# Kernel tuning notes

Measured on AMD Instinct MI355X. Metric: run time of the kernel, lower is better.

The kernel has to match this reference:

```python
import jax, jax.numpy as jnp
import numpy as np

B, L, HID, H, D = 1, 2048, 3072, 24, 128
MLP = 4 * HID
LH, LW = 32, 56      # latent mask grid -> LH*LW image tokens at the END of the sequence
LIP = 16             # IP-adapter image tokens
IP_SCALE = 0.6


def setup_inputs() -> dict:
    key = jax.random.key(0)
    k = jax.random.split(key, 10)
    # Flux rotary pe layout [1,1,L,D//2,2,2]: pe[...,0]=[cos,-sin], pe[...,1]=[sin,cos]
    pos = jnp.arange(L, dtype=jnp.float32)
    freqs = 1.0 / (10000.0 ** (jnp.arange(0, D, 2, dtype=jnp.float32) / D))
    ang = pos[:, None] * freqs[None, :]            # [L, D//2]
    cos, sin = jnp.cos(ang), jnp.sin(ang)
    pe = jnp.stack([jnp.stack([cos, -sin], -1), jnp.stack([sin, cos], -1)], -2)[None, None]
    return {
        "x": jax.random.normal(k[0], (B, L, HID), jnp.float32),
        "vec": jax.random.normal(k[1], (B, HID), jnp.float32),
        "pe": pe,
        "img_mask": jax.random.uniform(k[2], (B, LH, LW), jnp.float32),
        "image_emb": jax.random.normal(k[3], (B, LIP, HID), jnp.float32),
        "mod_w": jax.random.normal(k[4], (3 * HID, HID), jnp.float32) * 0.02,
        "mod_b": jnp.zeros((3 * HID,), jnp.float32),
        "lin1_w": jax.random.normal(k[5], (3 * HID + MLP, HID), jnp.float32) * 0.02,
        "lin1_b": jnp.zeros((3 * HID + MLP,), jnp.float32),
        "q_scale": jnp.ones((D,), jnp.float32),
        "k_scale": jnp.ones((D,), jnp.float32),
        "lin2_w": jax.random.normal(k[6], (HID, HID + MLP), jnp.float32) * 0.02,
        "lin2_b": jnp.zeros((HID,), jnp.float32),
        "ipk_w": jax.random.normal(k[7], (HID, HID), jnp.float32) * 0.02,
        "ipv_w": jax.random.normal(k[8], (HID, HID), jnp.float32) * 0.02,
    }


def _rms(x, scale, eps):
    # RMSNorm over last dim (QKNorm / norm_added_k)
    return x * jax.lax.rsqrt(jnp.mean(x * x, -1, keepdims=True) + eps) * scale


def _apply_rope(x, pe):
    # x: [B,H,L,D]; pe: [1,1,L,D//2,2,2]
    xr = x.reshape(x.shape[:-1] + (D // 2, 1, 2))
    out = pe[..., 0] * xr[..., 0] + pe[..., 1] * xr[..., 1]  # [B,H,L,D//2,2]
    return out.reshape(x.shape)


def _sdpa(q, k, v):
    # q:[B,H,Lq,D] k,v:[B,H,Lk,D] -> [B,Lq,H*D]
    s = jnp.einsum('bhqd,bhkd->bhqk', q, k) / jnp.sqrt(jnp.float32(D))
    o = jnp.einsum('bhqk,bhkd->bhqd', jax.nn.softmax(s, -1), v)
    return o.transpose(0, 2, 1, 3).reshape(q.shape[0], q.shape[2], H * D)


def reference(x, vec, pe, img_mask, image_emb, mod_w, mod_b, lin1_w, lin1_b,
              q_scale, k_scale, lin2_w, lin2_b, ipk_w, ipv_w):
    # modulation: SiLU(vec) -> Linear -> (shift, scale, gate), each [B,1,HID]
    mod = jax.nn.silu(vec) @ mod_w.T + mod_b
    shift, scale, gate = [m[:, None, :] for m in jnp.split(mod, 3, -1)]
    # pre_norm: LayerNorm, no affine, eps 1e-6 (biased variance, matches torch)
    ln = (x - jnp.mean(x, -1, keepdims=True)) * jax.lax.rsqrt(jnp.var(x, -1, keepdims=True) + 1e-6)
    x_mod = (1.0 + scale) * ln + shift
    # fused qkv + mlp projection
    h = x_mod @ lin1_w.T + lin1_b
    qkv, mlp = h[..., :3 * HID], h[..., 3 * HID:]
    q, k, v = qkv.reshape(B, L, 3, H, D).transpose(2, 0, 3, 1, 4)  # each [B,H,L,D]
    q = _rms(q, q_scale, 1e-6)
    k = _rms(k, k_scale, 1e-6)
    # rp_attention: RoPE then SDPA
    attn = _sdpa(_apply_rope(q, pe), _apply_rope(k, pe), v)       # [B,L,HID]
    # IP-adapter cross-attention: pre-rope q attends to projected image_emb
    ip_k = _rms((image_emb @ ipk_w.T).reshape(B, LIP, H, D).transpose(0, 2, 1, 3), 1.0, 1e-5)
    ip_v = (image_emb @ ipv_w.T).reshape(B, LIP, H, D).transpose(0, 2, 1, 3)
    ip_h = IP_SCALE * _sdpa(q, ip_k, ip_v)                        # [B,L,HID]
    # spatial mask applied to last LH*LW tokens, zeros elsewhere
    full_mask = jnp.concatenate(
        [jnp.zeros((B, L - LH * LW), ip_h.dtype), img_mask.reshape(B, LH * LW)], 1)
    attn = attn + ip_h * full_mask[..., None]
    out = jnp.concatenate([attn, jax.nn.gelu(mlp, approximate=True)], -1) @ lin2_w.T + lin2_b
    return x + gate * out
```

## Files before the change

### kernel.cpp

```cpp
#include <hip/hip_runtime.h>

#define HID 3072
#define LSEQ 2048
#define NH 24
#define HD 128
#define N1 21504
#define K2 15360

typedef unsigned short ushort_t;
typedef __attribute__((ext_vector_type(8))) short bf16x8;
typedef __attribute__((ext_vector_type(4))) float f32x4;

__device__ __forceinline__ unsigned short f2bf(float f) {
    union { float f; unsigned int u; } v; v.f = f;
    unsigned int u = v.u;
    u += 0x7fffu + ((u >> 16) & 1u);
    return (unsigned short)(u >> 16);
}
__device__ __forceinline__ float bf2f(unsigned short s) {
    union { unsigned int u; float f; } v; v.u = ((unsigned int)s) << 16;
    return v.f;
}
__device__ __forceinline__ float gelu_tanh(float x) {
    float u = 0.7978845608028654f * (x + 0.044715f * x * x * x);
    float t = 2.0f / (1.0f + __expf(-2.0f * u)) - 1.0f;
    return 0.5f * x * (1.0f + t);
}
__device__ __forceinline__ void gload_lds16(const ushort_t* g, ushort_t* l) {
    __builtin_amdgcn_global_load_lds((const __attribute__((address_space(1))) void*)g,
                                     (__attribute__((address_space(3))) void*)l, 16, 0, 0);
}

__global__ __launch_bounds__(256) void k_cvt(const float* __restrict__ src,
    ushort_t* __restrict__ dst, int n)
{
    int stride = gridDim.x * 256 * 8;
    for (int i = (blockIdx.x * 256 + threadIdx.x) * 8; i < n; i += stride) {
        float4 a = *reinterpret_cast<const float4*>(src + i);
        float4 b = *reinterpret_cast<const float4*>(src + i + 4);
        uint4 pk;
        pk.x = (unsigned)f2bf(a.x) | ((unsigned)f2bf(a.y) << 16);
        pk.y = (unsigned)f2bf(a.z) | ((unsigned)f2bf(a.w) << 16);
        pk.z = (unsigned)f2bf(b.x) | ((unsigned)f2bf(b.y) << 16);
        pk.w = (unsigned)f2bf(b.z) | ((unsigned)f2bf(b.w) << 16);
        *reinterpret_cast<uint4*>(dst + i) = pk;
    }
}

__global__ __launch_bounds__(256) void k_mod(const float* __restrict__ vec,
    const float* __restrict__ mw, const float* __restrict__ mb, float* __restrict__ mod) {
    __shared__ __align__(16) float sv[HID];
    int tid = threadIdx.x;
    for (int i = tid; i < HID; i += 256) {
        float v = vec[i];
        sv[i] = v / (1.0f + __expf(-v));
    }
    __syncthreads();
    int wave = tid >> 6, lane = tid & 63;
    int n = blockIdx.x * 4 + wave;
    const float* w = mw + (size_t)n * HID;
    float acc = 0.0f;
    for (int k = lane * 4; k < HID; k += 256) {
        float4 wv = *reinterpret_cast<const float4*>(w + k);
        float4 s  = *reinterpret_cast<const float4*>(sv + k);
        acc += wv.x * s.x + wv.y * s.y + wv.z * s.z + wv.w * s.w;
    }
    #pragma unroll
    for (int off = 1; off < 64; off <<= 1) acc += __shfl_xor(acc, off);
    if (lane == 0) mod[n] = acc + mb[n];
}

__global__ __launch_bounds__(256) void k_lnmod(const float* __restrict__ x,
    const float* __restrict__ mod, ushort_t* __restrict__ xmod) {
    int row = blockIdx.x, tid = threadIdx.x;
    const float4* xr = reinterpret_cast<const float4*>(x + (size_t)row * HID);
    float4 v[3];
    float s = 0.f, sq = 0.f;
    #pragma unroll
    for (int i = 0; i < 3; ++i) {
        v[i] = xr[tid + i * 256];
        s  += v[i].x + v[i].y + v[i].z + v[i].w;
        sq += v[i].x * v[i].x + v[i].y * v[i].y + v[i].z * v[i].z + v[i].w * v[i].w;
    }
    #pragma unroll
    for (int off = 1; off < 64; off <<= 1) { s += __shfl_xor(s, off); sq += __shfl_xor(sq, off); }
    __shared__ float rs[4], rq[4];
    int wave = tid >> 6, lane = tid & 63;
    if (lane == 0) { rs[wave] = s; rq[wave] = sq; }
    __syncthreads();
    s  = rs[0] + rs[1] + rs[2] + rs[3];
    sq = rq[0] + rq[1] + rq[2] + rq[3];
    float mean = s * (1.0f / HID);
    float var = sq * (1.0f / HID) - mean * mean;
    float rstd = rsqrtf(var + 1e-6f);
    ushort_t* orow = xmod + (size_t)row * HID;
    #pragma unroll
    for (int i = 0; i < 3; ++i) {
        int c = (tid + i * 256) * 4;
        float4 sc = *reinterpret_cast<const float4*>(mod + HID + c);
        float4 sh = *reinterpret_cast<const float4*>(mod + c);
        float o0 = (1.f + sc.x) * ((v[i].x - mean) * rstd) + sh.x;
        float o1 = (1.f + sc.y) * ((v[i].y - mean) * rstd) + sh.y;
        float o2 = (1.f + sc.z) * ((v[i].z - mean) * rstd) + sh.z;
        float o3 = (1.f + sc.w) * ((v[i].w - mean) * rstd) + sh.w;
        *reinterpret_cast<ushort4*>(orow + c) = make_ushort4(f2bf(o0), f2bf(o1), f2bf(o2), f2bf(o3));
    }
}

#define MFMA_CLUSTER(PH, AF)                                                          \
    do {                                                                              \
        __builtin_amdgcn_s_setprio(1);                                                \
        _Pragma("unroll") for (int i_ = 0; i_ < 2; ++i_)                              \
        _Pragma("unroll") for (int nj_ = 0; nj_ < 4; ++nj_)                           \
        _Pragma("unroll") for (int kh_ = 0; kh_ < 2; ++kh_)                           \
            acc[2 * (PH) + i_][nj_] = __builtin_amdgcn_mfma_f32_16x16x32_bf16(        \
                AF[i_][kh_], bfrag[nj_][kh_], acc[2 * (PH) + i_][nj_], 0, 0, 0);      \
        __builtin_amdgcn_s_setprio(0);                                                \
    } while (0)

template<int EPI>
__global__ __launch_bounds__(512) void k_gemm8(
    const ushort_t* __restrict__ A, const ushort_t* __restrict__ W,
    const float* __restrict__ bias, int Ks, int klen,
    ushort_t* __restrict__ out_qkv, ushort_t* __restrict__ out_concat,
    float* __restrict__ part)
{
    extern __shared__ __align__(16) char smem_raw[];
    ushort_t* smem = (ushort_t*)smem_raw;
    int tid = threadIdx.x;
    int wid = tid >> 6, l = tid & 63;
    int wm = wid >> 2, wn = wid & 3;
    int lr = l & 15, lg = l >> 4;

    int NTILE = (EPI == 1) ? 84 : 12;
    int flat = blockIdx.y * NTILE + blockIdx.x;
    int nf = (flat & 7) * NTILE + (flat >> 3);
    int mt = nf & 7, nt = nf >> 3;
    int m0 = mt * 256, n0 = nt * 256;
    int koff = blockIdx.z * klen;
    int NT = klen >> 6;

    int lrow = l >> 3;
    int lc   = (l & 7) ^ lrow;
    int arow_st = wm * 128 + wn * 32 + lrow;
    int bhalf = wn >> 1, ridx = wm * 2 + (wn & 1);
    int brow_st = bhalf * 128 + ridx * 32 + lrow;
    const ushort_t* aSrc = A + (size_t)(m0 + arow_st) * Ks + koff + lc * 8;
    const ushort_t* bSrc = W + (size_t)(n0 + brow_st) * Ks + koff + lc * 8;
    int aDst = (wm * 128 + wn * 32) * 64;
    int bDst = (bhalf * 128 + ridx * 32) * 64;

    auto stageA = [&](int t, int buf, int c) {
        gload_lds16(aSrc + (size_t)c * 8 * Ks + (size_t)t * 64,
                    smem + buf * 16384 + aDst + c * 512);
    };
    auto stageB = [&](int t, int c) {
        gload_lds16(bSrc + (size_t)c * 8 * Ks + (size_t)t * 64,
                    smem + 49152 + (t & 1) * 16384 + bDst + c * 512);
    };
    auto readA = [&](int buf, int row, int ccc) {
        return *reinterpret_cast<const bf16x8*>(smem + buf * 16384 + row * 64 + ((ccc ^ (row & 7)) << 3));
    };
    auto readB = [&](int p, int row, int ccc) {
        return *reinterpret_cast<const bf16x8*>(smem + 49152 + p * 16384 + row * 64 + ((ccc ^ (row & 7)) << 3));
    };

    f32x4 acc[8][4] = {};

    #pragma unroll
    for (int c = 0; c < 4; ++c) stageA(0, 0, c);
    #pragma unroll
    for (int c = 0; c < 4; ++c) stageB(0, c);
    #pragma unroll
    for (int c = 0; c < 4; ++c) stageA(1, 1, c);
    #pragma unroll
    for (int c = 0; c < 4; ++c) stageB(1, c);
    asm volatile("s_waitcnt vmcnt(8)" ::: "memory");
    __builtin_amdgcn_s_barrier();

    int pA = 0;
    int pA2 = 2;
    for (int t = 0; t < NT; ++t) {
        int pB = t & 1;
        bf16x8 bfrag[4][2], af0[2][2], af1[2][2], af2[2][2], af3[2][2];
        #pragma unroll
        for (int nj = 0; nj < 4; ++nj)
            #pragma unroll
            for (int kh = 0; kh < 2; ++kh)
                bfrag[nj][kh] = readB(pB, wn * 64 + nj * 16 + lr, kh * 4 + lg);
        #pragma unroll
        for (int i = 0; i < 2; ++i)
            #pragma unroll
            for (int kh = 0; kh < 2; ++kh)
                af0[i][kh] = readA(pA, wm * 128 + i * 16 + lr, kh * 4 + lg);
        if (t + 2 < NT) {
            stageA(t + 2, pA2, 0); stageA(t + 2, pA2, 1);
            stageA(t + 2, pA2, 2); stageA(t + 2, pA2, 3);
        }
        #pragma unroll
        for (int i = 0; i < 2; ++i)
            #pragma unroll
            for (int kh = 0; kh < 2; ++kh)
                af1[i][kh] = readA(pA, wm * 128 + (2 + i) * 16 + lr, kh * 4 + lg);
        MFMA_CLUSTER(0, af0);
        #pragma unroll
        for (int i = 0; i < 2; ++i)
            #pragma unroll
            for (int kh = 0; kh < 2; ++kh)
                af2[i][kh] = readA(pA, wm * 128 + (4 + i) * 16 + lr, kh * 4 + lg);
        MFMA_CLUSTER(1, af1);
        __builtin_amdgcn_s_barrier();
        if (t + 2 < NT) {
            stageB(t + 2, 0); stageB(t + 2, 1);
            stageB(t + 2, 2); stageB(t + 2, 3);
        }
        #pragma unroll
        for (int i = 0; i < 2; ++i)
            #pragma unroll
            for (int kh = 0; kh < 2; ++kh)
                af3[i][kh] = readA(pA, wm * 128 + (6 + i) * 16 + lr, kh * 4 + lg);
        MFMA_CLUSTER(2, af2);
        MFMA_CLUSTER(3, af3);
        if (t + 2 < NT)      asm volatile("s_waitcnt vmcnt(8)" ::: "memory");
        else if (t + 1 < NT) asm volatile("s_waitcnt vmcnt(0)" ::: "memory");
        __builtin_amdgcn_s_barrier();
        pA  = (pA  + 1 == 3) ? 0 : pA  + 1;
        pA2 = (pA2 + 1 == 3) ? 0 : pA2 + 1;
    }

    #pragma unroll
    for (int nj = 0; nj < 4; ++nj) {
        int col = n0 + wn * 64 + nj * 16 + lr;
        float b = (EPI == 1) ? bias[col] : 0.f;
        #pragma unroll
        for (int mi = 0; mi < 8; ++mi) {
            int rbase = m0 + wm * 128 + mi * 16 + lg * 4;
            #pragma unroll
            for (int r = 0; r < 4; ++r) {
                int mrow = rbase + r;
                float val = acc[mi][nj][r] + b;
                if (EPI == 1) {
                    if (col < 3 * HID) {
                        out_qkv[(size_t)mrow * (3 * HID) + col] = f2bf(val);
                    } else {
                        out_concat[(size_t)mrow * K2 + HID + (col - 3 * HID)] = f2bf(gelu_tanh(val));
                    }
                } else {
                    part[(size_t)blockIdx.z * LSEQ * HID + (size_t)mrow * HID + col] = val;
                }
            }
        }
    }
}

__global__ __launch_bounds__(256) void k_red(const float* __restrict__ part,
    const float* __restrict__ bias, const float* __restrict__ xres,
    const float* __restrict__ mod, float* __restrict__ dout)
{
    size_t base = ((size_t)blockIdx.x * 256 + threadIdx.x) * 4;
    int col = (int)(base % HID);
    float4 s = *reinterpret_cast<const float4*>(part + base);
    #pragma unroll
    for (int z = 1; z < 8; ++z) {
        float4 p = *reinterpret_cast<const float4*>(part + (size_t)z * LSEQ * HID + base);
        s.x += p.x; s.y += p.y; s.z += p.z; s.w += p.w;
    }
    float4 bb = *reinterpret_cast<const float4*>(bias + col);
    float4 gg = *reinterpret_cast<const float4*>(mod + 2 * HID + col);
    float4 xx = *reinterpret_cast<const float4*>(xres + base);
    float4 o;
    o.x = xx.x + gg.x * (s.x + bb.x);
    o.y = xx.y + gg.y * (s.y + bb.y);
    o.z = xx.z + gg.z * (s.z + bb.z);
    o.w = xx.w + gg.w * (s.w + bb.w);
    *reinterpret_cast<float4*>(dout + base) = o;
}

__global__ __launch_bounds__(256) void k_qkv(const ushort_t* __restrict__ qkv,
    const float* __restrict__ pe, const float* __restrict__ q_scale, const float* __restrict__ k_scale,
    ushort_t* __restrict__ q_rope, ushort_t* __restrict__ k_rope,
    ushort_t* __restrict__ q_rms, ushort_t* __restrict__ v_t)
{
    __shared__ ushort_t vtile[64][132];
    int h = blockIdx.y, l0 = blockIdx.x * 64;
    int wave = threadIdx.x >> 6, lane = threadIdx.x & 63;
    int d0 = lane * 2;
    float qs0 = q_scale[d0], qs1 = q_scale[d0 + 1];
    float ks0 = k_scale[d0], ks1 = k_scale[d0 + 1];
    for (int it = 0; it < 16; ++it) {
        int ll = it * 4 + wave;
        int l = l0 + ll;
        const ushort_t* base = qkv + (size_t)l * (3 * HID) + h * HD + d0;
        unsigned qw = *reinterpret_cast<const unsigned*>(base);
        unsigned kw = *reinterpret_cast<const unsigned*>(base + HID);
        unsigned vw = *reinterpret_cast<const unsigned*>(base + 2 * HID);
        float qx = bf2f((ushort_t)(qw & 0xffffu)), qy = bf2f((ushort_t)(qw >> 16));
        float kx = bf2f((ushort_t)(kw & 0xffffu)), ky = bf2f((ushort_t)(kw >> 16));
        float sq = qx * qx + qy * qy;
        float sk = kx * kx + ky * ky;
        #pragma unroll
        for (int off = 1; off < 64; off <<= 1) { sq += __shfl_xor(sq, off); sk += __shfl_xor(sk, off); }
        float rqv = rsqrtf(sq * (1.0f / HD) + 1e-6f);
        float rkv = rsqrtf(sk * (1.0f / HD) + 1e-6f);
        float qnx = qx * rqv * qs0, qny = qy * rqv * qs1;
        float knx = kx * rkv * ks0, kny = ky * rkv * ks1;
        float4 p = *reinterpret_cast<const float4*>(pe + ((size_t)l * 64 + lane) * 4);
        size_t off_hl = ((size_t)h * LSEQ + l) * HD + d0;
        *reinterpret_cast<unsigned*>(q_rms + off_hl) = (unsigned)f2bf(qnx) | ((unsigned)f2bf(qny) << 16);
        float qrx = p.x * qnx + p.y * qny, qry = p.z * qnx + p.w * qny;
        float krx = p.x * knx + p.y * kny, kry = p.z * knx + p.w * kny;
        *reinterpret_cast<unsigned*>(q_rope + off_hl) = (unsigned)f2bf(qrx) | ((unsigned)f2bf(qry) << 16);
        *reinterpret_cast<unsigned*>(k_rope + off_hl) = (unsigned)f2bf(krx) | ((unsigned)f2bf(kry) << 16);
        vtile[ll][d0] = (ushort_t)(vw & 0xffffu);
        vtile[ll][d0 + 1] = (ushort_t)(vw >> 16);
    }
    __syncthreads();
    int d = threadIdx.x >> 1, half = threadIdx.x & 1;
    ushort_t* dst = v_t + ((size_t)h * HD + d) * LSEQ + l0 + half * 32;
    #pragma unroll
    for (int g = 0; g < 4; ++g) {
        unsigned w0, w1, w2, w3;
        int lb = half * 32 + g * 8;
        w0 = (unsigned)vtile[lb + 0][d] | ((unsigned)vtile[lb + 1][d] << 16);
        w1 = (unsigned)vtile[lb + 2][d] | ((unsigned)vtile[lb + 3][d] << 16);
        w2 = (unsigned)vtile[lb + 4][d] | ((unsigned)vtile[lb + 5][d] << 16);
        w3 = (unsigned)vtile[lb + 6][d] | ((unsigned)vtile[lb + 7][d] << 16);
        reinterpret_cast<uint4*>(dst)[g] = make_uint4(w0, w1, w2, w3);
    }
}

__global__ __launch_bounds__(256) void k_ipgemv(const float* __restrict__ emb,
    const float* __restrict__ wk, const float* __restrict__ wv,
    float* __restrict__ ipk, float* __restrict__ ipv)
{
    int task = blockIdx.x * 4 + (threadIdx.x >> 6);
    int lane = threadIdx.x & 63;
    int which = task / HID;
    int n = task % HID;
    const float* w = (which ? wv : wk) + (size_t)n * HID;
    float acc[16];
    #pragma unroll
    for (int t = 0; t < 16; ++t) acc[t] = 0.f;
    for (int k = lane; k < HID; k += 64) {
        float wval = w[k];
        #pragma unroll
        for (int t = 0; t < 16; ++t) acc[t] += emb[t * HID + k] * wval;
    }
    #pragma unroll
    for (int off = 1; off < 64; off <<= 1) {
        #pragma unroll
        for (int t = 0; t < 16; ++t) acc[t] += __shfl_xor(acc[t], off);
    }
    if (lane == 0) {
        int hh = n >> 7, d = n & 127;
        float* dstp = which ? ipv : ipk;
        #pragma unroll
        for (int t = 0; t < 16; ++t) dstp[((size_t)hh * 16 + t) * HD + d] = acc[t];
    }
}

__global__ __launch_bounds__(256) void k_ipkrms(float* __restrict__ ipk) {
    int row = blockIdx.x * 4 + (threadIdx.x >> 6);
    int lane = threadIdx.x & 63;
    float2 v = *reinterpret_cast<const float2*>(ipk + (size_t)row * HD + lane * 2);
    float sq = v.x * v.x + v.y * v.y;
    #pragma unroll
    for (int off = 1; off < 64; off <<= 1) sq += __shfl_xor(sq, off);
    float r = rsqrtf(sq * (1.0f / HD) + 1e-5f);
    float2 o; o.x = v.x * r; o.y = v.y * r;
    *reinterpret_cast<float2*>(ipk + (size_t)row * HD + lane * 2) = o;
}

__global__ __launch_bounds__(256) void k_attn(const ushort_t* __restrict__ q_rope,
    const ushort_t* __restrict__ k_rope, const ushort_t* __restrict__ v_t,
    float* __restrict__ attnbuf)
{
    __shared__ __align__(16) ushort_t Ks[32 * 128];
    __shared__ __align__(16) ushort_t Vs[128 * 32];
    __shared__ __align__(16) ushort_t Ps[4 * 32 * 40];
    const float SC = 0.08838834764831845f;
    int h = blockIdx.y, q0 = blockIdx.x * 128;
    int tid = threadIdx.x, wave = tid >> 6, lane = tid & 63;
    int lr = lane & 15, lg = lane >> 4;
    const ushort_t* Kb = k_rope + (size_t)h * LSEQ * HD;
    const ushort_t* Vb = v_t + (size_t)h * HD * LSEQ;
    bf16x8 qf[2][4];
    #pragma unroll
    for (int i = 0; i < 2; ++i) {
        #pragma unroll
        for (int ks = 0; ks < 4; ++ks) {
            int row = q0 + wave * 32 + i * 16 + lr;
            int d = ks * 32 + lg * 8;
            qf[i][ks] = *reinterpret_cast<const bf16x8*>(q_rope + ((size_t)h * LSEQ + row) * HD + d);
        }
    }
    f32x4 o[2][8] = {};
    float mrun[2][4], lrun[2][4];
    #pragma unroll
    for (int i = 0; i < 2; ++i)
        #pragma unroll
        for (int r = 0; r < 4; ++r) { mrun[i][r] = -1e30f; lrun[i][r] = 0.f; }

    for (int kt = 0; kt < LSEQ; kt += 32) {
        #pragma unroll
        for (int ii = 0; ii < 2; ++ii) {
            int c = tid + ii * 256;
            int krow = c >> 4, kc = c & 15;
            uint4 va = *reinterpret_cast<const uint4*>(Kb + (size_t)(kt + krow) * HD + kc * 8);
            *reinterpret_cast<uint4*>(reinterpret_cast<char*>(Ks) + krow * 256 + ((kc ^ (krow & 15)) << 4)) = va;
            int dr = c >> 2, vc = c & 3;
            uint4 vb = *reinterpret_cast<const uint4*>(Vb + (size_t)dr * LSEQ + kt + vc * 8);
            *reinterpret_cast<uint4*>(reinterpret_cast<char*>(Vs) + dr * 64 + ((vc ^ ((dr >> 1) & 3)) << 4)) = vb;
        }
        __syncthreads();
        f32x4 s[2][2] = {};
        #pragma unroll
        for (int ks = 0; ks < 4; ++ks) {
            bf16x8 kf[2];
            #pragma unroll
            for (int j = 0; j < 2; ++j) {
                int krow = j * 16 + lr;
                int cc = ks * 4 + lg;
                kf[j] = *reinterpret_cast<const bf16x8*>(reinterpret_cast<char*>(Ks) + krow * 256 + ((cc ^ (krow & 15)) << 4));
            }
            #pragma unroll
            for (int i = 0; i < 2; ++i)
                #pragma unroll
                for (int j = 0; j < 2; ++j)
                    s[i][j] = __builtin_amdgcn_mfma_f32_16x16x32_bf16(qf[i][ks], kf[j], s[i][j], 0, 0, 0);
        }
        float alpha[2][4];
        #pragma unroll
        for (int i = 0; i < 2; ++i) {
            #pragma unroll
            for (int r = 0; r < 4; ++r) {
                float v0 = s[i][0][r] * SC, v1 = s[i][1][r] * SC;
                float mx = fmaxf(v0, v1);
                #pragma unroll
                for (int off = 1; off < 16; off <<= 1) mx = fmaxf(mx, __shfl_xor(mx, off));
                float mnew = fmaxf(mrun[i][r], mx);
                float al = __expf(mrun[i][r] - mnew);
                float p0 = __expf(v0 - mnew), p1 = __expf(v1 - mnew);
                float rs2 = p0 + p1;
                #pragma unroll
                for (int off = 1; off < 16; off <<= 1) rs2 += __shfl_xor(rs2, off);
                lrun[i][r] = lrun[i][r] * al + rs2;
                mrun[i][r] = mnew;
                alpha[i][r] = al;
                s[i][0][r] = p0; s[i][1][r] = p1;
            }
        }
        #pragma unroll
        for (int i = 0; i < 2; ++i)
            #pragma unroll
            for (int j8 = 0; j8 < 8; ++j8)
                #pragma unroll
                for (int r = 0; r < 4; ++r) o[i][j8][r] *= alpha[i][r];
        #pragma unroll
        for (int i = 0; i < 2; ++i)
            #pragma unroll
            for (int j = 0; j < 2; ++j)
                #pragma unroll
                for (int r = 0; r < 4; ++r) {
                    int ql = i * 16 + lg * 4 + r;
                    int kp = j * 16 + lr;
                    Ps[wave * 1280 + ql * 40 + kp] = f2bf(s[i][j][r]);
                }
        __syncthreads();
        bf16x8 pa[2];
        #pragma unroll
        for (int i = 0; i < 2; ++i)
            pa[i] = *reinterpret_cast<const bf16x8*>(Ps + wave * 1280 + (i * 16 + lr) * 40 + lg * 8);
        #pragma unroll
        for (int j8 = 0; j8 < 8; ++j8) {
            int d = j8 * 16 + lr;
            bf16x8 vf = *reinterpret_cast<const bf16x8*>(reinterpret_cast<char*>(Vs) + d * 64 + ((lg ^ ((d >> 1) & 3)) << 4));
            #pragma unroll
            for (int i = 0; i < 2; ++i)
                o[i][j8] = __builtin_amdgcn_mfma_f32_16x16x32_bf16(pa[i], vf, o[i][j8], 0, 0, 0);
        }
        __syncthreads();
    }
    #pragma unroll
    for (int i = 0; i < 2; ++i) {
        #pragma unroll
        for (int r = 0; r < 4; ++r) {
            float inv = 1.0f / lrun[i][r];
            int mrow = q0 + wave * 32 + i * 16 + lg * 4 + r;
            float* orow = attnbuf + (size_t)mrow * HID + h * HD;
            #pragma unroll
            for (int j8 = 0; j8 < 8; ++j8)
                orow[j8 * 16 + lr] = o[i][j8][r] * inv;
        }
    }
}

__global__ __launch_bounds__(256) void k_ipattn(const ushort_t* __restrict__ q_rms,
    const float* __restrict__ ipk, const float* __restrict__ ipv,
    const float* __restrict__ attnbuf, const float* __restrict__ img_mask,
    ushort_t* __restrict__ concat)
{
    int task = blockIdx.x * 4 + (threadIdx.x >> 6);
    int lane = threadIdx.x & 63;
    int h = task >> 11;
    int l = task & 2047;
    int d0 = lane * 2;
    float2 a = *reinterpret_cast<const float2*>(attnbuf + (size_t)l * HID + h * HD + d0);
    if (l >= 256) {
        float mask = img_mask[l - 256];
        unsigned qv = *reinterpret_cast<const unsigned*>(q_rms + ((size_t)h * LSEQ + l) * HD + d0);
        float qx = bf2f((unsigned short)(qv & 0xffffu)), qy = bf2f((unsigned short)(qv >> 16));
        float s[16];
        const float* kb = ipk + (size_t)h * 16 * HD + d0;
        #pragma unroll
        for (int j = 0; j < 16; ++j) {
            float2 kk = *reinterpret_cast<const float2*>(kb + j * HD);
            float part = qx * kk.x + qy * kk.y;
            #pragma unroll
            for (int off = 1; off < 64; off <<= 1) part += __shfl_xor(part, off);
            s[j] = part * 0.08838834764831845f;
        }
        float mx = s[0];
        #pragma unroll
        for (int j = 1; j < 16; ++j) mx = fmaxf(mx, s[j]);
        float sum = 0.f;
        #pragma unroll
        for (int j = 0; j < 16; ++j) { s[j] = __expf(s[j] - mx); sum += s[j]; }
        float ox = 0.f, oy = 0.f;
        const float* vb = ipv + (size_t)h * 16 * HD + d0;
        #pragma unroll
        for (int j = 0; j < 16; ++j) {
            float2 vv = *reinterpret_cast<const float2*>(vb + j * HD);
            ox += s[j] * vv.x; oy += s[j] * vv.y;
        }
        float f = 0.6f * mask / sum;
        a.x += f * ox; a.y += f * oy;
    }
    *reinterpret_cast<unsigned*>(concat + (size_t)l * K2 + h * HD + d0) =
        (unsigned)f2bf(a.x) | ((unsigned)f2bf(a.y) << 16);
}

extern "C" void kernel_launch(void* const* d_in, const int* in_sizes, int n_in,
                              void* d_out, int out_size, void* d_ws, size_t ws_size,
                              hipStream_t stream)
{
    (void)in_sizes; (void)n_in; (void)out_size; (void)ws_size;
    const float* x         = (const float*)d_in[0];
    const float* vec       = (const float*)d_in[1];
    const float* pe        = (const float*)d_in[2];
    const float* img_mask  = (const float*)d_in[3];
    const float* image_emb = (const float*)d_in[4];
    const float* mod_w     = (const float*)d_in[5];
    const float* mod_b     = (const float*)d_in[6];
    const float* lin1_w    = (const float*)d_in[7];
    const float* lin1_b    = (const float*)d_in[8];
    const float* q_scale   = (const float*)d_in[9];
    const float* k_scale   = (const float*)d_in[10];
    const float* lin2_w    = (const float*)d_in[11];
    const float* lin2_b    = (const float*)d_in[12];
    const float* ipk_w     = (const float*)d_in[13];
    const float* ipv_w     = (const float*)d_in[14];
    float* dout = (float*)d_out;

    char* wp = (char*)d_ws;
    auto alloc = [&](size_t bytes) { char* p = wp; wp += (bytes + 255) & ~(size_t)255; return p; };
    float*    mod     = (float*)   alloc((size_t)9216 * 4);
    ushort_t* concat  = (ushort_t*)alloc((size_t)LSEQ * K2 * 2);
    ushort_t* lin2_bf = (ushort_t*)alloc((size_t)HID * K2 * 2);
    float*    ipk     = (float*)   alloc((size_t)NH * 16 * HD * 4);
    float*    ipv     = (float*)   alloc((size_t)NH * 16 * HD * 4);
    char* ubase = wp;
    ushort_t* lin1_bf = (ushort_t*)alloc((size_t)N1 * HID * 2);
    ushort_t* xmod    = (ushort_t*)alloc((size_t)LSEQ * HID * 2);
    ushort_t* qkv     = (ushort_t*)alloc((size_t)LSEQ * 3 * HID * 2);
    float*    attnbuf = (float*)   alloc((size_t)LSEQ * HID * 4);
    ushort_t* q_rope  = (ushort_t*)alloc((size_t)NH * LSEQ * HD * 2);
    ushort_t* k_rope  = (ushort_t*)alloc((size_t)NH * LSEQ * HD * 2);
    ushort_t* q_rms   = (ushort_t*)alloc((size_t)NH * LSEQ * HD * 2);
    ushort_t* v_t     = (ushort_t*)alloc((size_t)NH * HD * LSEQ * 2);
    float*    partial = (float*)ubase;

    hipFuncSetAttribute((const void*)k_gemm8<1>, hipFuncAttributeMaxDynamicSharedMemorySize, 163840);
    hipFuncSetAttribute((const void*)k_gemm8<0>, hipFuncAttributeMaxDynamicSharedMemorySize, 163840);

    k_cvt   <<<dim3(2048), dim3(256), 0, stream>>>(lin1_w, lin1_bf, N1 * HID);
    k_cvt   <<<dim3(2048), dim3(256), 0, stream>>>(lin2_w, lin2_bf, HID * K2);
    k_mod   <<<dim3(9216 / 4), dim3(256), 0, stream>>>(vec, mod_w, mod_b, mod);
    k_lnmod <<<dim3(LSEQ), dim3(256), 0, stream>>>(x, mod, xmod);
    k_gemm8<1><<<dim3(84, 8, 1), dim3(512), 163840, stream>>>(xmod, lin1_bf, lin1_b, HID, HID,
                                                              qkv, concat, nullptr);
    k_qkv   <<<dim3(32, NH), dim3(256), 0, stream>>>(qkv, pe, q_scale, k_scale,
                                                     q_rope, k_rope, q_rms, v_t);
    k_ipgemv<<<dim3(2 * HID / 4), dim3(256), 0, stream>>>(image_emb, ipk_w, ipv_w, ipk, ipv);
    k_ipkrms<<<dim3(NH * 16 / 4), dim3(256), 0, stream>>>(ipk);
    k_attn  <<<dim3(16, NH), dim3(256), 0, stream>>>(q_rope, k_rope, v_t, attnbuf);
    k_ipattn<<<dim3(NH * LSEQ / 4), dim3(256), 0, stream>>>(q_rms, ipk, ipv, attnbuf, img_mask, concat);
    k_gemm8<0><<<dim3(12, 8, 8), dim3(512), 163840, stream>>>(concat, lin2_bf, nullptr, K2, 1920,
                                                              nullptr, nullptr, partial);
    k_red   <<<dim3(LSEQ * HID / 1024), dim3(256), 0, stream>>>(partial, lin2_b, x, mod, dout);
}
```

Baseline: 1.160 ms.

## Widen attention key tile, fuse weight conversions, halve lin2 split-K factor

Attention now processes 64 keys per iteration instead of 32, with larger LDS tiles, a new V swizzle and s_setprio around the MFMA sections. This halves the number of barrier-separated iterations and amortizes softmax bookkeeping, at the cost of more registers and LDS. The two fp32-to-bf16 weight conversions are merged into one launch. The lin2 GEMM split-K goes from 8 to 4 slices, which halves partial-sum traffic in the reduction but also halves the grid's parallelism.

New measurement: 1.069 ms. 1.09x faster.

```diff
diff --git a/kernel.cpp b/kernel.cpp
--- a/kernel.cpp
+++ b/kernel.cpp
@@ -31,19 +31,31 @@
                                      (__attribute__((address_space(3))) void*)l, 16, 0, 0);
 }
 
-__global__ __launch_bounds__(256) void k_cvt(const float* __restrict__ src,
-    ushort_t* __restrict__ dst, int n)
+__global__ __launch_bounds__(256) void k_cvt2(const float* __restrict__ s1,
+    ushort_t* __restrict__ d1, int n1, const float* __restrict__ s2,
+    ushort_t* __restrict__ d2, int n2)
 {
     int stride = gridDim.x * 256 * 8;
-    for (int i = (blockIdx.x * 256 + threadIdx.x) * 8; i < n; i += stride) {
-        float4 a = *reinterpret_cast<const float4*>(src + i);
-        float4 b = *reinterpret_cast<const float4*>(src + i + 4);
+    int base = (blockIdx.x * 256 + threadIdx.x) * 8;
+    for (int i = base; i < n1; i += stride) {
+        float4 a = *reinterpret_cast<const float4*>(s1 + i);
+        float4 b = *reinterpret_cast<const float4*>(s1 + i + 4);
         uint4 pk;
         pk.x = (unsigned)f2bf(a.x) | ((unsigned)f2bf(a.y) << 16);
         pk.y = (unsigned)f2bf(a.z) | ((unsigned)f2bf(a.w) << 16);
         pk.z = (unsigned)f2bf(b.x) | ((unsigned)f2bf(b.y) << 16);
         pk.w = (unsigned)f2bf(b.z) | ((unsigned)f2bf(b.w) << 16);
-        *reinterpret_cast<uint4*>(dst + i) = pk;
+        *reinterpret_cast<uint4*>(d1 + i) = pk;
+    }
+    for (int i = base; i < n2; i += stride) {
+        float4 a = *reinterpret_cast<const float4*>(s2 + i);
+        float4 b = *reinterpret_cast<const float4*>(s2 + i + 4);
+        uint4 pk;
+        pk.x = (unsigned)f2bf(a.x) | ((unsigned)f2bf(a.y) << 16);
+        pk.y = (unsigned)f2bf(a.z) | ((unsigned)f2bf(a.w) << 16);
+        pk.z = (unsigned)f2bf(b.x) | ((unsigned)f2bf(b.y) << 16);
+        pk.w = (unsigned)f2bf(b.z) | ((unsigned)f2bf(b.w) << 16);
+        *reinterpret_cast<uint4*>(d2 + i) = pk;
     }
 }
 
@@ -261,7 +273,7 @@
     int col = (int)(base % HID);
     float4 s = *reinterpret_cast<const float4*>(part + base);
     #pragma unroll
-    for (int z = 1; z < 8; ++z) {
+    for (int z = 1; z < 4; ++z) {
         float4 p = *reinterpret_cast<const float4*>(part + (size_t)z * LSEQ * HID + base);
         s.x += p.x; s.y += p.y; s.z += p.z; s.w += p.w;
     }
@@ -375,9 +387,9 @@
     const ushort_t* __restrict__ k_rope, const ushort_t* __restrict__ v_t,
     float* __restrict__ attnbuf)
 {
-    __shared__ __align__(16) ushort_t Ks[32 * 128];
-    __shared__ __align__(16) ushort_t Vs[128 * 32];
-    __shared__ __align__(16) ushort_t Ps[4 * 32 * 40];
+    __shared__ __align__(16) ushort_t Ks[64 * 128];
+    __shared__ __align__(16) ushort_t Vs[128 * 64];
+    __shared__ __align__(16) ushort_t Ps[4 * 32 * 72];
     const float SC = 0.08838834764831845f;
     int h = blockIdx.y, q0 = blockIdx.x * 128;
     int tid = threadIdx.x, wave = tid >> 6, lane = tid & 63;
@@ -401,24 +413,25 @@
         #pragma unroll
         for (int r = 0; r < 4; ++r) { mrun[i][r] = -1e30f; lrun[i][r] = 0.f; }
 
-    for (int kt = 0; kt < LSEQ; kt += 32) {
-        #pragma unroll
-        for (int ii = 0; ii < 2; ++ii) {
+    for (int kt = 0; kt < LSEQ; kt += 64) {
+        #pragma unroll
+        for (int ii = 0; ii < 4; ++ii) {
             int c = tid + ii * 256;
             int krow = c >> 4, kc = c & 15;
             uint4 va = *reinterpret_cast<const uint4*>(Kb + (size_t)(kt + krow) * HD + kc * 8);
             *reinterpret_cast<uint4*>(reinterpret_cast<char*>(Ks) + krow * 256 + ((kc ^ (krow & 15)) << 4)) = va;
-            int dr = c >> 2, vc = c & 3;
+            int dr = c >> 3, vc = c & 7;
             uint4 vb = *reinterpret_cast<const uint4*>(Vb + (size_t)dr * LSEQ + kt + vc * 8);
-            *reinterpret_cast<uint4*>(reinterpret_cast<char*>(Vs) + dr * 64 + ((vc ^ ((dr >> 1) & 3)) << 4)) = vb;
+            *reinterpret_cast<uint4*>(reinterpret_cast<char*>(Vs) + dr * 128 + ((vc ^ (dr & 7)) << 4)) = vb;
         }
         __syncthreads();
-        f32x4 s[2][2] = {};
+        f32x4 s[2][4] = {};
+        __builtin_amdgcn_s_setprio(1);
         #pragma unroll
         for (int ks = 0; ks < 4; ++ks) {
-            bf16x8 kf[2];
-            #pragma unroll
-            for (int j = 0; j < 2; ++j) {
+            bf16x8 kf[4];
+            #pragma unroll
+            for (int j = 0; j < 4; ++j) {
                 int krow = j * 16 + lr;
                 int cc = ks * 4 + lg;
                 kf[j] = *reinterpret_cast<const bf16x8*>(reinterpret_cast<char*>(Ks) + krow * 256 + ((cc ^ (krow & 15)) << 4));
@@ -426,28 +439,31 @@
             #pragma unroll
             for (int i = 0; i < 2; ++i)
                 #pragma unroll
-                for (int j = 0; j < 2; ++j)
+                for (int j = 0; j < 4; ++j)
                     s[i][j] = __builtin_amdgcn_mfma_f32_16x16x32_bf16(qf[i][ks], kf[j], s[i][j], 0, 0, 0);
         }
+        __builtin_amdgcn_s_setprio(0);
         float alpha[2][4];
         #pragma unroll
         for (int i = 0; i < 2; ++i) {
             #pragma unroll
             for (int r = 0; r < 4; ++r) {
                 float v0 = s[i][0][r] * SC, v1 = s[i][1][r] * SC;
-                float mx = fmaxf(v0, v1);
+                float v2 = s[i][2][r] * SC, v3 = s[i][3][r] * SC;
+                float mx = fmaxf(fmaxf(v0, v1), fmaxf(v2, v3));
                 #pragma unroll
                 for (int off = 1; off < 16; off <<= 1) mx = fmaxf(mx, __shfl_xor(mx, off));
                 float mnew = fmaxf(mrun[i][r], mx);
                 float al = __expf(mrun[i][r] - mnew);
                 float p0 = __expf(v0 - mnew), p1 = __expf(v1 - mnew);
-                float rs2 = p0 + p1;
+                float p2 = __expf(v2 - mnew), p3 = __expf(v3 - mnew);
+                float rs2 = p0 + p1 + p2 + p3;
                 #pragma unroll
                 for (int off = 1; off < 16; off <<= 1) rs2 += __shfl_xor(rs2, off);
                 lrun[i][r] = lrun[i][r] * al + rs2;
                 mrun[i][r] = mnew;
                 alpha[i][r] = al;
-                s[i][0][r] = p0; s[i][1][r] = p1;
+                s[i][0][r] = p0; s[i][1][r] = p1; s[i][2][r] = p2; s[i][3][r] = p3;
             }
         }
         #pragma unroll
@@ -459,26 +475,34 @@
         #pragma unroll
         for (int i = 0; i < 2; ++i)
             #pragma unroll
-            for (int j = 0; j < 2; ++j)
+            for (int j = 0; j < 4; ++j)
                 #pragma unroll
                 for (int r = 0; r < 4; ++r) {
                     int ql = i * 16 + lg * 4 + r;
                     int kp = j * 16 + lr;
-                    Ps[wave * 1280 + ql * 40 + kp] = f2bf(s[i][j][r]);
+                    Ps[wave * 2304 + ql * 72 + kp] = f2bf(s[i][j][r]);
                 }
         __syncthreads();
-        bf16x8 pa[2];
+        bf16x8 pa[2][2];
         #pragma unroll
         for (int i = 0; i < 2; ++i)
-            pa[i] = *reinterpret_cast<const bf16x8*>(Ps + wave * 1280 + (i * 16 + lr) * 40 + lg * 8);
+            #pragma unroll
+            for (int ks2 = 0; ks2 < 2; ++ks2)
+                pa[i][ks2] = *reinterpret_cast<const bf16x8*>(Ps + wave * 2304 + (i * 16 + lr) * 72 + ks2 * 32 + lg * 8);
+        __builtin_amdgcn_s_setprio(1);
         #pragma unroll
         for (int j8 = 0; j8 < 8; ++j8) {
             int d = j8 * 16 + lr;
-            bf16x8 vf = *reinterpret_cast<const bf16x8*>(reinterpret_cast<char*>(Vs) + d * 64 + ((lg ^ ((d >> 1) & 3)) << 4));
-            #pragma unroll
-            for (int i = 0; i < 2; ++i)
-                o[i][j8] = __builtin_amdgcn_mfma_f32_16x16x32_bf16(pa[i], vf, o[i][j8], 0, 0, 0);
-        }
+            #pragma unroll
+            for (int ks2 = 0; ks2 < 2; ++ks2) {
+                int cc = ks2 * 4 + lg;
+                bf16x8 vf = *reinterpret_cast<const bf16x8*>(reinterpret_cast<char*>(Vs) + d * 128 + ((cc ^ (d & 7)) << 4));
+                #pragma unroll
+                for (int i = 0; i < 2; ++i)
+                    o[i][j8] = __builtin_amdgcn_mfma_f32_16x16x32_bf16(pa[i][ks2], vf, o[i][j8], 0, 0, 0);
+            }
+        }
+        __builtin_amdgcn_s_setprio(0);
         __syncthreads();
     }
     #pragma unroll
@@ -583,8 +607,8 @@
     hipFuncSetAttribute((const void*)k_gemm8<1>, hipFuncAttributeMaxDynamicSharedMemorySize, 163840);
     hipFuncSetAttribute((const void*)k_gemm8<0>, hipFuncAttributeMaxDynamicSharedMemorySize, 163840);
 
-    k_cvt   <<<dim3(2048), dim3(256), 0, stream>>>(lin1_w, lin1_bf, N1 * HID);
-    k_cvt   <<<dim3(2048), dim3(256), 0, stream>>>(lin2_w, lin2_bf, HID * K2);
+    k_cvt2  <<<dim3(4096), dim3(256), 0, stream>>>(lin1_w, lin1_bf, N1 * HID,
+                                                   lin2_w, lin2_bf, HID * K2);
     k_mod   <<<dim3(9216 / 4), dim3(256), 0, stream>>>(vec, mod_w, mod_b, mod);
     k_lnmod <<<dim3(LSEQ), dim3(256), 0, stream>>>(x, mod, xmod);
     k_gemm8<1><<<dim3(84, 8, 1), dim3(512), 163840, stream>>>(xmod, lin1_bf, lin1_b, HID, HID,
@@ -595,7 +619,7 @@
     k_ipkrms<<<dim3(NH * 16 / 4), dim3(256), 0, stream>>>(ipk);
     k_attn  <<<dim3(16, NH), dim3(256), 0, stream>>>(q_rope, k_rope, v_t, attnbuf);
     k_ipattn<<<dim3(NH * LSEQ / 4), dim3(256), 0, stream>>>(q_rms, ipk, ipv, attnbuf, img_mask, concat);
-    k_gemm8<0><<<dim3(12, 8, 8), dim3(512), 163840, stream>>>(concat, lin2_bf, nullptr, K2, 1920,
+    k_gemm8<0><<<dim3(12, 8, 4), dim3(512), 163840, stream>>>(concat, lin2_bf, nullptr, K2, 3840,
                                                               nullptr, nullptr, partial);
     k_red   <<<dim3(LSEQ * HID / 1024), dim3(256), 0, stream>>>(partial, lin2_b, x, mod, dout);
 }
```
